# Kernel tuning notes

Measured on AMD Instinct MI355X. Metric: run time of the kernel, lower is better.

The kernel has to match this reference:

```python
import jax, jax.numpy as jnp
import numpy as np

B, F, D = 4096, 32, 32
LAYER_SIZE = [128, 128]


def setup_inputs() -> dict:
    key = jax.random.key(0)
    k1, k2, k3 = jax.random.split(key, 3)
    inputs = jax.random.normal(k1, (B, F, D), dtype=jnp.float32)
    # CIN filters: shape [1, field_nums[0]*field_nums[i], field_nums[i+1]]
    field_nums = [F] + LAYER_SIZE
    filter_0 = (jax.random.normal(k2, (1, field_nums[0] * field_nums[0], field_nums[1]), dtype=jnp.float32) * 0.05)
    filter_1 = (jax.random.normal(k3, (1, field_nums[0] * field_nums[1], field_nums[2]), dtype=jnp.float32) * 0.05)
    return {"inputs": inputs, "filter_0": filter_0, "filter_1": filter_1}


def _cin_forward(inputs, filters):
    x0 = inputs          # [B, F, D] -- hidden_nn_layers[0]
    prev = inputs        # hidden_nn_layers[-1]
    outs = []
    for W in filters:    # W: [1, F*M, N]
        # outer product over field dims: [B, F, M, D]
        z = jnp.einsum('bhd,bmd->bhmd', x0, prev)
        b, h, m, d = z.shape
        z = z.reshape(b, h * m, d)                 # [B, F*M, D]
        # 1x1 conv over the F*M axis == contraction with W[0]: [F*M, N]
        cur = jnp.einsum('bpd,pn->bnd', z, W[0])   # [B, N, D]
        cur = jax.nn.relu(cur)
        prev = cur
        outs.append(cur)
    result = jnp.concatenate(outs, axis=1)         # [B, sum(layer_size), D]
    return jnp.sum(result, axis=-1)                # [B, sum(layer_size)]


def reference(inputs, filter_0, filter_1):
    return _cin_forward(inputs, (filter_0, filter_1))
```

## Files before the change

### kernel.cpp

```cpp
#include <hip/hip_runtime.h>


typedef _Float16 half_t;
typedef _Float16 half4v __attribute__((ext_vector_type(4)));
typedef _Float16 half8 __attribute__((ext_vector_type(8)));
typedef float f32x16 __attribute__((ext_vector_type(16)));

__global__ void prep_w_kernel(const float* __restrict__ W0,
                              const float* __restrict__ W1,
                              half_t* __restrict__ Wp0,
                              half_t* __restrict__ Wp1) {
  int gid = blockIdx.x * 256 + threadIdx.x;
  int n = gid & 127;
  int tg = (gid >> 7) & 1;
  int s = gid >> 8;
  const float* W;
  half_t* Wp;
  int M, sl;
  if (s < 64) { W = W0; Wp = Wp0; M = 32; sl = s; }
  else        { W = W1; Wp = Wp1; M = 128; sl = s - 64; }
  int h = sl & 31, mc = sl >> 5;
  int kbase = h * M + mc * 16 + tg * 8;
  half8 v;
#pragma unroll
  for (int j = 0; j < 8; ++j) v[j] = (half_t)W[(size_t)(kbase + j) * 128 + n];
  *(half8*)(Wp + ((size_t)(sl * 2 + tg) * 128 + n) * 8) = v;
}

__device__ __forceinline__ int pswz(int row, int m) {
  return row * 128 + (((m >> 3) ^ (row & 15)) << 3) + (m & 7);
}

__device__ __forceinline__ f32x16 mfma3216(half8 a, half8 b, f32x16 c) {
  return __builtin_amdgcn_mfma_f32_32x32x16_f16(a, b, c, 0, 0, 0);
}

template <int MC, bool L1>
__device__ __forceinline__ void layer_loop(const half_t* __restrict__ Wp,
                                           const half_t* __restrict__ psrc,
                                           const half_t* __restrict__ xQw,
                                           int woff0, int woff1, int rowb,
                                           int l31, int hi, f32x16 acc[2][2]) {
  half8 P[2];
#pragma unroll
  for (int rt = 0; rt < 2; ++rt)
    P[rt] = L1 ? *(const half8*)&psrc[(rowb + rt * 32 + l31) * 40 + hi * 8]
               : *(const half8*)&psrc[pswz(rowb + rt * 32 + l31, hi * 8)];

#pragma unroll 1
  for (int mc = 0; mc < MC; ++mc) {
#pragma unroll 1
    for (int p = 0; p < 8; ++p) {
      const int sb = mc * 32 + 4 * p;
      half8 xq = *(const half8*)(xQw + p * 256);
      {
        half8 B00 = *(const half8*)(Wp + (size_t)(sb + 0) * 2048 + woff0);
        half8 B01 = *(const half8*)(Wp + (size_t)(sb + 0) * 2048 + woff1);
        half8 B10 = *(const half8*)(Wp + (size_t)(sb + 1) * 2048 + woff0);
        half8 B11 = *(const half8*)(Wp + (size_t)(sb + 1) * 2048 + woff1);
        half8 A00 = P[0] * xq[0];
        half8 A10 = P[1] * xq[2];
        half8 A01 = P[0] * xq[1];
        half8 A11 = P[1] * xq[3];
        acc[0][0] = mfma3216(A00, B00, acc[0][0]);
        acc[0][1] = mfma3216(A00, B01, acc[0][1]);
        acc[1][0] = mfma3216(A10, B00, acc[1][0]);
        acc[1][1] = mfma3216(A10, B01, acc[1][1]);
        acc[0][0] = mfma3216(A01, B10, acc[0][0]);
        acc[0][1] = mfma3216(A01, B11, acc[0][1]);
        acc[1][0] = mfma3216(A11, B10, acc[1][0]);
        acc[1][1] = mfma3216(A11, B11, acc[1][1]);
      }
      {
        half8 B00 = *(const half8*)(Wp + (size_t)(sb + 2) * 2048 + woff0);
        half8 B01 = *(const half8*)(Wp + (size_t)(sb + 2) * 2048 + woff1);
        half8 B10 = *(const half8*)(Wp + (size_t)(sb + 3) * 2048 + woff0);
        half8 B11 = *(const half8*)(Wp + (size_t)(sb + 3) * 2048 + woff1);
        half8 A00 = P[0] * xq[4];
        half8 A10 = P[1] * xq[6];
        half8 A01 = P[0] * xq[5];
        half8 A11 = P[1] * xq[7];
        acc[0][0] = mfma3216(A00, B00, acc[0][0]);
        acc[0][1] = mfma3216(A00, B01, acc[0][1]);
        acc[1][0] = mfma3216(A10, B00, acc[1][0]);
        acc[1][1] = mfma3216(A10, B01, acc[1][1]);
        acc[0][0] = mfma3216(A01, B10, acc[0][0]);
        acc[0][1] = mfma3216(A01, B11, acc[0][1]);
        acc[1][0] = mfma3216(A11, B10, acc[1][0]);
        acc[1][1] = mfma3216(A11, B11, acc[1][1]);
      }
    }
    if (mc + 1 < MC) {
      const int mn = (mc + 1) * 16;
#pragma unroll
      for (int rt = 0; rt < 2; ++rt)
        P[rt] = L1 ? *(const half8*)&psrc[(rowb + rt * 32 + l31) * 40 + mn +
                                          hi * 8]
                   : *(const half8*)&psrc[pswz(rowb + rt * 32 + l31,
                                               mn + hi * 8)];
    }
  }
}

__global__ __launch_bounds__(256, 4) void cin_fused_kernel(
    const float* __restrict__ x0,
    const half_t* __restrict__ Wp0,
    const half_t* __restrict__ Wp1,
    float* __restrict__ out) {
  __shared__ half_t xQ[2 * 8 * 32 * 8];
  __shared__ half_t prevT[4 * 32 * 128];
  half_t* xT = prevT;

  const int tid = threadIdx.x;
  const int b0 = blockIdx.x * 4;

  const float4* x4 = (const float4*)(x0 + (size_t)b0 * 1024);
#pragma unroll
  for (int r = 0; r < 4; ++r) {
    int q = r * 256 + tid;
    float4 v = x4[q];
    int e4 = q * 4;
    int bi = e4 >> 10, h = (e4 >> 5) & 31, d0 = e4 & 31;
    half4v hv = {(half_t)v.x, (half_t)v.y, (half_t)v.z, (half_t)v.w};
    const int pair = bi >> 1, rtl = bi & 1;
    const int pp = h >> 2, hpar = (h >> 1) & 1, par = h & 1;
#pragma unroll
    for (int j = 0; j < 4; ++j) {
      xQ[pair * 2048 + pp * 256 + (d0 + j) * 8 + hpar * 4 + rtl * 2 + par] =
          hv[j];
      xT[(bi * 32 + d0 + j) * 40 + h] = hv[j];
    }
  }
  __syncthreads();

  const int lane = tid & 63;
  const int l31 = lane & 31;
  const int hi = lane >> 5;
  const int wave = tid >> 6;
  const int wr = wave >> 1;
  const int wc = wave & 1;

  const int woff0 = hi * 1024 + (wc * 64 + l31) * 8;
  const int woff1 = hi * 1024 + (wc * 64 + 32 + l31) * 8;
  const int rowb = wr * 64;
  const half_t* xQw = xQ + wr * 2048 + l31 * 8;

  f32x16 acc[2][2];
#pragma unroll
  for (int rt = 0; rt < 2; ++rt)
#pragma unroll
    for (int ct = 0; ct < 2; ++ct)
#pragma unroll
      for (int r = 0; r < 16; ++r) acc[rt][ct][r] = 0.f;

  layer_loop<2, true>(Wp0, xT, xQw, woff0, woff1, rowb, l31, hi, acc);

  __syncthreads();

#pragma unroll
  for (int rt = 0; rt < 2; ++rt) {
#pragma unroll
    for (int ct = 0; ct < 2; ++ct) {
      float s = 0.f;
#pragma unroll
      for (int r = 0; r < 16; ++r) {
        float v = acc[rt][ct][r];
        v = v > 0.f ? v : 0.f;
        s += v;
        int d = (r & 3) + ((r >> 2) << 3) + hi * 4;
        prevT[pswz(rowb + rt * 32 + d, wc * 64 + ct * 32 + l31)] = (half_t)v;
        acc[rt][ct][r] = 0.f;
      }
      s += __shfl_down(s, 32);
      if (lane < 32)
        out[(size_t)(b0 + wr * 2 + rt) * 256 + wc * 64 + ct * 32 + lane] = s;
    }
  }
  __syncthreads();

  layer_loop<8, false>(Wp1, prevT, xQw, woff0, woff1, rowb, l31, hi, acc);

#pragma unroll
  for (int rt = 0; rt < 2; ++rt) {
#pragma unroll
    for (int ct = 0; ct < 2; ++ct) {
      float s = 0.f;
#pragma unroll
      for (int r = 0; r < 16; ++r) {
        float v = acc[rt][ct][r];
        s += v > 0.f ? v : 0.f;
      }
      s += __shfl_down(s, 32);
      if (lane < 32)
        out[(size_t)(b0 + wr * 2 + rt) * 256 + 128 + wc * 64 + ct * 32 +
            lane] = s;
    }
  }
}

extern "C" void kernel_launch(void* const* d_in, const int* in_sizes, int n_in,
                              void* d_out, int out_size, void* d_ws,
                              size_t ws_size, hipStream_t stream) {
  const float* x0 = (const float*)d_in[0];
  const float* w0 = (const float*)d_in[1];
  const float* w1 = (const float*)d_in[2];
  float* out = (float*)d_out;
  char* ws = (char*)d_ws;

  half_t* Wp0 = (half_t*)(ws);
  half_t* Wp1 = (half_t*)(ws + 64 * 2048 * 2);

  hipLaunchKernelGGL(prep_w_kernel, dim3(320), dim3(256), 0, stream, w0, w1,
                     Wp0, Wp1);
  hipLaunchKernelGGL(cin_fused_kernel, dim3(1024), dim3(256), 0, stream, x0,
                     Wp0, Wp1, out);
}
```

Before: 230.8 us.

## Process eight batch rows per block with per-wave column tiles and prefetched weights

Each block now handles 8 batch elements instead of 4. Each wave owns one 32-column output tile across all 8 row tiles, which quadruples reuse of every loaded weight fragment across MFMAs. The weight B-operand loads are software-prefetched one step ahead in rotating registers. The cost is 8 accumulators of 16 floats per lane and double the LDS, so launch bounds drop to 2 blocks per CU and the grid halves, which lowers occupancy and parallelism.

```diff
diff --git a/kernel.cpp b/kernel.cpp
--- a/kernel.cpp
+++ b/kernel.cpp
@@ -38,96 +38,88 @@
 template <int MC, bool L1>
 __device__ __forceinline__ void layer_loop(const half_t* __restrict__ Wp,
                                            const half_t* __restrict__ psrc,
-                                           const half_t* __restrict__ xQw,
-                                           int woff0, int woff1, int rowb,
-                                           int l31, int hi, f32x16 acc[2][2]) {
-  half8 P[2];
+                                           const half_t* __restrict__ xQb,
+                                           int woff, int l31, int hi,
+                                           f32x16 acc[8]) {
+  half8 P[8];
 #pragma unroll
-  for (int rt = 0; rt < 2; ++rt)
-    P[rt] = L1 ? *(const half8*)&psrc[(rowb + rt * 32 + l31) * 40 + hi * 8]
-               : *(const half8*)&psrc[pswz(rowb + rt * 32 + l31, hi * 8)];
+  for (int rt = 0; rt < 8; ++rt)
+    P[rt] = L1 ? *(const half8*)&psrc[(rt * 32 + l31) * 40 + hi * 8]
+               : *(const half8*)&psrc[pswz(rt * 32 + l31, hi * 8)];
+
+  half8 Br0 = *(const half8*)(Wp + (size_t)0 * 2048 + woff);
+  half8 Br1 = *(const half8*)(Wp + (size_t)1 * 2048 + woff);
+  half8 Br2 = *(const half8*)(Wp + (size_t)2 * 2048 + woff);
+  half8 Br3 = *(const half8*)(Wp + (size_t)3 * 2048 + woff);
 
 #pragma unroll 1
   for (int mc = 0; mc < MC; ++mc) {
 #pragma unroll 1
     for (int p = 0; p < 8; ++p) {
-      const int sb = mc * 32 + 4 * p;
-      half8 xq = *(const half8*)(xQw + p * 256);
-      {
-        half8 B00 = *(const half8*)(Wp + (size_t)(sb + 0) * 2048 + woff0);
-        half8 B01 = *(const half8*)(Wp + (size_t)(sb + 0) * 2048 + woff1);
-        half8 B10 = *(const half8*)(Wp + (size_t)(sb + 1) * 2048 + woff0);
-        half8 B11 = *(const half8*)(Wp + (size_t)(sb + 1) * 2048 + woff1);
-        half8 A00 = P[0] * xq[0];
-        half8 A10 = P[1] * xq[2];
-        half8 A01 = P[0] * xq[1];
-        half8 A11 = P[1] * xq[3];
-        acc[0][0] = mfma3216(A00, B00, acc[0][0]);
-        acc[0][1] = mfma3216(A00, B01, acc[0][1]);
-        acc[1][0] = mfma3216(A10, B00, acc[1][0]);
-        acc[1][1] = mfma3216(A10, B01, acc[1][1]);
-        acc[0][0] = mfma3216(A01, B10, acc[0][0]);
-        acc[0][1] = mfma3216(A01, B11, acc[0][1]);
-        acc[1][0] = mfma3216(A11, B10, acc[1][0]);
-        acc[1][1] = mfma3216(A11, B11, acc[1][1]);
-      }
-      {
-        half8 B00 = *(const half8*)(Wp + (size_t)(sb + 2) * 2048 + woff0);
-        half8 B01 = *(const half8*)(Wp + (size_t)(sb + 2) * 2048 + woff1);
-        half8 B10 = *(const half8*)(Wp + (size_t)(sb + 3) * 2048 + woff0);
-        half8 B11 = *(const half8*)(Wp + (size_t)(sb + 3) * 2048 + woff1);
-        half8 A00 = P[0] * xq[4];
-        half8 A10 = P[1] * xq[6];
-        half8 A01 = P[0] * xq[5];
-        half8 A11 = P[1] * xq[7];
-        acc[0][0] = mfma3216(A00, B00, acc[0][0]);
-        acc[0][1] = mfma3216(A00, B01, acc[0][1]);
-        acc[1][0] = mfma3216(A10, B00, acc[1][0]);
-        acc[1][1] = mfma3216(A10, B01, acc[1][1]);
-        acc[0][0] = mfma3216(A01, B10, acc[0][0]);
-        acc[0][1] = mfma3216(A01, B11, acc[0][1]);
-        acc[1][0] = mfma3216(A11, B10, acc[1][0]);
-        acc[1][1] = mfma3216(A11, B11, acc[1][1]);
-      }
+      const int h0 = p * 4;
+      const int sb = mc * 32 + h0;
+      half8 xq0 = *(const half8*)(xQb + (h0 + 0) * 256);
+      half8 xq1 = *(const half8*)(xQb + (h0 + 1) * 256);
+      half8 xq2 = *(const half8*)(xQb + (h0 + 2) * 256);
+      half8 xq3 = *(const half8*)(xQb + (h0 + 3) * 256);
+
+#define SSTEP(XQ, BR, OFFJ)                                               \
+  {                                                                       \
+    half8 A0 = P[0] * XQ[0], A1 = P[1] * XQ[1], A2 = P[2] * XQ[2],        \
+          A3 = P[3] * XQ[3];                                              \
+    acc[0] = mfma3216(A0, BR, acc[0]);                                    \
+    acc[1] = mfma3216(A1, BR, acc[1]);                                    \
+    acc[2] = mfma3216(A2, BR, acc[2]);                                    \
+    acc[3] = mfma3216(A3, BR, acc[3]);                                    \
+    half8 A4 = P[4] * XQ[4], A5 = P[5] * XQ[5], A6 = P[6] * XQ[6],        \
+          A7 = P[7] * XQ[7];                                              \
+    acc[4] = mfma3216(A4, BR, acc[4]);                                    \
+    acc[5] = mfma3216(A5, BR, acc[5]);                                    \
+    acc[6] = mfma3216(A6, BR, acc[6]);                                    \
+    acc[7] = mfma3216(A7, BR, acc[7]);                                    \
+    BR = *(const half8*)(Wp +                                             \
+                         (size_t)((sb + 4 + OFFJ) & (MC * 32 - 1)) * 2048 \
+                         + woff);                                         \
+  }
+      SSTEP(xq0, Br0, 0)
+      SSTEP(xq1, Br1, 1)
+      SSTEP(xq2, Br2, 2)
+      SSTEP(xq3, Br3, 3)
+#undef SSTEP
     }
     if (mc + 1 < MC) {
       const int mn = (mc + 1) * 16;
 #pragma unroll
-      for (int rt = 0; rt < 2; ++rt)
-        P[rt] = L1 ? *(const half8*)&psrc[(rowb + rt * 32 + l31) * 40 + mn +
-                                          hi * 8]
-                   : *(const half8*)&psrc[pswz(rowb + rt * 32 + l31,
-                                               mn + hi * 8)];
+      for (int rt = 0; rt < 8; ++rt)
+        P[rt] = L1 ? *(const half8*)&psrc[(rt * 32 + l31) * 40 + mn + hi * 8]
+                   : *(const half8*)&psrc[pswz(rt * 32 + l31, mn + hi * 8)];
     }
   }
 }
 
-__global__ __launch_bounds__(256, 4) void cin_fused_kernel(
+__global__ __launch_bounds__(256, 2) void cin_fused_kernel(
     const float* __restrict__ x0,
     const half_t* __restrict__ Wp0,
     const half_t* __restrict__ Wp1,
     float* __restrict__ out) {
-  __shared__ half_t xQ[2 * 8 * 32 * 8];
-  __shared__ half_t prevT[4 * 32 * 128];
+  __shared__ half_t xQ[32 * 32 * 8];
+  __shared__ half_t prevT[8 * 32 * 128];
   half_t* xT = prevT;
 
   const int tid = threadIdx.x;
-  const int b0 = blockIdx.x * 4;
+  const int b0 = blockIdx.x * 8;
 
   const float4* x4 = (const float4*)(x0 + (size_t)b0 * 1024);
 #pragma unroll
-  for (int r = 0; r < 4; ++r) {
+  for (int r = 0; r < 8; ++r) {
     int q = r * 256 + tid;
     float4 v = x4[q];
     int e4 = q * 4;
     int bi = e4 >> 10, h = (e4 >> 5) & 31, d0 = e4 & 31;
     half4v hv = {(half_t)v.x, (half_t)v.y, (half_t)v.z, (half_t)v.w};
-    const int pair = bi >> 1, rtl = bi & 1;
-    const int pp = h >> 2, hpar = (h >> 1) & 1, par = h & 1;
 #pragma unroll
     for (int j = 0; j < 4; ++j) {
-      xQ[pair * 2048 + pp * 256 + (d0 + j) * 8 + hpar * 4 + rtl * 2 + par] =
-          hv[j];
+      xQ[(h * 32 + d0 + j) * 8 + bi] = hv[j];
       xT[(bi * 32 + d0 + j) * 40 + h] = hv[j];
     }
   }
@@ -137,64 +129,51 @@
   const int l31 = lane & 31;
   const int hi = lane >> 5;
   const int wave = tid >> 6;
-  const int wr = wave >> 1;
-  const int wc = wave & 1;
 
-  const int woff0 = hi * 1024 + (wc * 64 + l31) * 8;
-  const int woff1 = hi * 1024 + (wc * 64 + 32 + l31) * 8;
-  const int rowb = wr * 64;
-  const half_t* xQw = xQ + wr * 2048 + l31 * 8;
+  const int woff = hi * 1024 + (wave * 32 + l31) * 8;
+  const half_t* xQb = xQ + l31 * 8;
 
-  f32x16 acc[2][2];
+  f32x16 acc[8];
 #pragma unroll
-  for (int rt = 0; rt < 2; ++rt)
+  for (int rt = 0; rt < 8; ++rt)
 #pragma unroll
-    for (int ct = 0; ct < 2; ++ct)
-#pragma unroll
-      for (int r = 0; r < 16; ++r) acc[rt][ct][r] = 0.f;
+    for (int r = 0; r < 16; ++r) acc[rt][r] = 0.f;
 
-  layer_loop<2, true>(Wp0, xT, xQw, woff0, woff1, rowb, l31, hi, acc);
+  layer_loop<2, true>(Wp0, xT, xQb, woff, l31, hi, acc);
 
   __syncthreads();
 
 #pragma unroll
-  for (int rt = 0; rt < 2; ++rt) {
+  for (int rt = 0; rt < 8; ++rt) {
+    float s = 0.f;
 #pragma unroll
-    for (int ct = 0; ct < 2; ++ct) {
-      float s = 0.f;
-#pragma unroll
-      for (int r = 0; r < 16; ++r) {
-        float v = acc[rt][ct][r];
-        v = v > 0.f ? v : 0.f;
-        s += v;
-        int d = (r & 3) + ((r >> 2) << 3) + hi * 4;
-        prevT[pswz(rowb + rt * 32 + d, wc * 64 + ct * 32 + l31)] = (half_t)v;
-        acc[rt][ct][r] = 0.f;
-      }
-      s += __shfl_down(s, 32);
-      if (lane < 32)
-        out[(size_t)(b0 + wr * 2 + rt) * 256 + wc * 64 + ct * 32 + lane] = s;
+    for (int r = 0; r < 16; ++r) {
+      float v = acc[rt][r];
+      v = v > 0.f ? v : 0.f;
+      s += v;
+      int d = (r & 3) + ((r >> 2) << 3) + hi * 4;
+      prevT[pswz(rt * 32 + d, wave * 32 + l31)] = (half_t)v;
+      acc[rt][r] = 0.f;
     }
+    s += __shfl_down(s, 32);
+    if (lane < 32)
+      out[(size_t)(b0 + rt) * 256 + wave * 32 + lane] = s;
   }
   __syncthreads();
 
-  layer_loop<8, false>(Wp1, prevT, xQw, woff0, woff1, rowb, l31, hi, acc);
+  layer_loop<8, false>(Wp1, prevT, xQb, woff, l31, hi, acc);
 
 #pragma unroll
-  for (int rt = 0; rt < 2; ++rt) {
+  for (int rt = 0; rt < 8; ++rt) {
+    float s = 0.f;
 #pragma unroll
-    for (int ct = 0; ct < 2; ++ct) {
-      float s = 0.f;
-#pragma unroll
-      for (int r = 0; r < 16; ++r) {
-        float v = acc[rt][ct][r];
-        s += v > 0.f ? v : 0.f;
-      }
-      s += __shfl_down(s, 32);
-      if (lane < 32)
-        out[(size_t)(b0 + wr * 2 + rt) * 256 + 128 + wc * 64 + ct * 32 +
-            lane] = s;
+    for (int r = 0; r < 16; ++r) {
+      float v = acc[rt][r];
+      s += v > 0.f ? v : 0.f;
     }
+    s += __shfl_down(s, 32);
+    if (lane < 32)
+      out[(size_t)(b0 + rt) * 256 + 128 + wave * 32 + lane] = s;
   }
 }
 
@@ -212,6 +191,6 @@
 
   hipLaunchKernelGGL(prep_w_kernel, dim3(320), dim3(256), 0, stream, w0, w1,
                      Wp0, Wp1);
-  hipLaunchKernelGGL(cin_fused_kernel, dim3(1024), dim3(256), 0, stream, x0,
+  hipLaunchKernelGGL(cin_fused_kernel, dim3(512), dim3(256), 0, stream, x0,
                      Wp0, Wp1, out);
 }
```

Result: faster. 204.1 us (-11.6%).
